# Kernel tuning notes

Measured on AMD Instinct MI355X. Metric: run time of the kernel, lower is better.

## Reference

```python
import jax, jax.numpy as jnp
import numpy as np

TEMPERATURE = 1.0
IGNORE_INDEX = -100


def setup_inputs() -> dict:
    key = jax.random.key(0)
    k1, k2, k3 = jax.random.split(key, 3)
    N, V = 8192, 32000
    Q, D = 8192, 512
    return {
        "input": jax.random.normal(k1, (N, V), dtype=jnp.float32),
        "label": jax.random.randint(k2, (N,), 0, V, dtype=jnp.int64),
        "query": jax.random.normal(k3, (Q, D), dtype=jnp.float32),
    }


def _cross_entropy(logits, label):
    # nn.CrossEntropyLoss(ignore_index=IGNORE_INDEX): mean NLL over non-ignored.
    logp = jax.nn.log_softmax(logits, axis=-1)
    safe_label = jnp.clip(label, 0, logits.shape[-1] - 1)
    nll = -jnp.take_along_axis(logp, safe_label[:, None], axis=-1)[:, 0]
    valid = (label != IGNORE_INDEX)
    num_valid = jnp.maximum(jnp.sum(valid), 1)
    return jnp.sum(jnp.where(valid, nll, 0.0)) / num_valid.astype(logits.dtype)


def _query_similarity_penalty(query, temperature):
    sq_norm = jnp.sum(query * query, axis=-1)  # [Q]
    sq = sq_norm[:, None] + sq_norm[None, :] - 2.0 * (query @ query.T)
    sq = jnp.maximum(sq, 0.0)
    dist = jnp.sqrt(jnp.where(sq > 0.0, sq, 1.0))
    dist = jnp.where(sq > 0.0, dist, 0.0)  # exact 0 on diagonal
    sim = jnp.exp(-dist / temperature)
    return jnp.sqrt(jnp.sum(sim * sim))  # Frobenius norm


def reference(input, label, query):
    ce = _cross_entropy(input, label)
    penalty = _query_similarity_penalty(query, TEMPERATURE)
    return ce + penalty
```

## Files before the change

### kernel.cpp

```cpp
#include <hip/hip_runtime.h>
#include <hip/hip_bf16.h>
#include <cstdint>

typedef unsigned short u16;
typedef __attribute__((ext_vector_type(8))) short short8;
typedef __attribute__((ext_vector_type(4))) float floatx4;

#define IGNORE_INDEX (-100)

#define SIM_OFF 64
#define NLL_OFF 320
#define CNT_OFF 576

__global__ __launch_bounds__(256) void init_acc(float* acc) {
    for (int i = threadIdx.x; i < 1024; i += 256) acc[i] = 0.f;
}

__global__ __launch_bounds__(256) void prep_kernel(const float* __restrict__ q,
                                                   u16* __restrict__ qb,
                                                   float* __restrict__ nrm) {
    const int gwave = (blockIdx.x * 256 + threadIdx.x) >> 6;
    const int lane  = threadIdx.x & 63;
    const float4* src = (const float4*)(q + (size_t)gwave * 512);
    float4 a = src[lane * 2];
    float4 b = src[lane * 2 + 1];
    float v[8] = {a.x, a.y, a.z, a.w, b.x, b.y, b.z, b.w};
    float ss = 0.f;
    union { u16 u[8]; uint4 p; } pk;
#pragma unroll
    for (int t = 0; t < 8; ++t) {
        ss += v[t] * v[t];
        __hip_bfloat16 h = __float2bfloat16(v[t]);
        pk.u[t] = *(u16*)&h;
    }
    ((uint4*)qb)[(size_t)gwave * 64 + lane] = pk.p;
#pragma unroll
    for (int off = 32; off; off >>= 1) ss += __shfl_down(ss, off);
    if (lane == 0) nrm[gwave] = ss;
}

#define GLD16(g, l) __builtin_amdgcn_global_load_lds(                          \
    (const __attribute__((address_space(1))) void*)(g),                        \
    (__attribute__((address_space(3))) void*)(l), 16, 0, 0)

__global__ __launch_bounds__(256, 3) void fused_kernel(const u16* __restrict__ qb,
                                                       const float* __restrict__ nrm,
                                                       const float* __restrict__ x,
                                                       const int* __restrict__ lab,
                                                       float* __restrict__ accs,
                                                       int V, int N, int tiles_per_side) {
    __shared__ __align__(16) u16 At[128 * 64];
    __shared__ __align__(16) u16 Bt[128 * 64];
    __shared__ float red[4];
    const int bid  = blockIdx.x;
    const int tid  = threadIdx.x;
    const int lane = tid & 63;
    const int w    = tid >> 6;
    const int slot = (bid & 63) * 4;

    if (bid % 5 == 0) {
        int t = bid / 5;
        int ti = 0, rem = t;
        while (rem >= tiles_per_side - ti) { rem -= tiles_per_side - ti; ++ti; }
        const int tj = ti + rem;
        const int i0 = ti * 128;
        const int j0 = tj * 128;
        const int wr = w >> 1, wc = w & 1;
        const int m15 = lane & 15, quad = lane >> 4;

        floatx4 acc[4][4];
#pragma unroll
        for (int a = 0; a < 4; ++a)
#pragma unroll
            for (int b = 0; b < 4; ++b) acc[a][b] = (floatx4)0.f;

        for (int kt = 0; kt < 8; ++kt) {
            const int k0 = kt * 64;
#pragma unroll
            for (int it = 0; it < 4; ++it) {
                int c   = it * 256 + tid;
                int row = c >> 3;
                int kc  = (c & 7) ^ (row & 7);
                const u16* ga = qb + (size_t)(i0 + row) * 512 + k0 + kc * 8;
                const u16* gb = qb + (size_t)(j0 + row) * 512 + k0 + kc * 8;
                GLD16(ga, &At[c * 8]);
                GLD16(gb, &Bt[c * 8]);
            }
            __syncthreads();
#pragma unroll
            for (int ks = 0; ks < 2; ++ks) {
                const int kcq = ks * 4 + quad;
                short8 af[4], bfr[4];
#pragma unroll
                for (int f = 0; f < 4; ++f) {
                    int ra = wr * 64 + f * 16 + m15;
                    af[f]  = *(const short8*)&At[(ra * 8 + (kcq ^ (ra & 7))) * 8];
                    int rb = wc * 64 + f * 16 + m15;
                    bfr[f] = *(const short8*)&Bt[(rb * 8 + (kcq ^ (rb & 7))) * 8];
                }
#pragma unroll
                for (int fi = 0; fi < 4; ++fi)
#pragma unroll
                    for (int fj = 0; fj < 4; ++fj)
                        acc[fi][fj] = __builtin_amdgcn_mfma_f32_16x16x32_bf16(
                            af[fi], bfr[fj], acc[fi][fj], 0, 0, 0);
            }
            __syncthreads();
        }

        float ni[4][4], nj[4];
#pragma unroll
        for (int fi = 0; fi < 4; ++fi)
#pragma unroll
            for (int r = 0; r < 4; ++r)
                ni[fi][r] = nrm[i0 + wr * 64 + fi * 16 + quad * 4 + r];
#pragma unroll
        for (int fj = 0; fj < 4; ++fj) nj[fj] = nrm[j0 + wc * 64 + fj * 16 + m15];

        float lsum = 0.f;
#pragma unroll
        for (int fi = 0; fi < 4; ++fi) {
#pragma unroll
            for (int fj = 0; fj < 4; ++fj) {
#pragma unroll
                for (int r = 0; r < 4; ++r) {
                    int i = i0 + wr * 64 + fi * 16 + quad * 4 + r;
                    int j = j0 + wc * 64 + fj * 16 + m15;
                    float sq = ni[fi][r] + nj[fj] - 2.f * acc[fi][fj][r];
                    float s;
                    if (i == j) s = 1.f;
                    else if (sq > 0.f) s = __expf(-sqrtf(sq));
                    else s = 1.f;
                    lsum += s * s;
                }
            }
        }
#pragma unroll
        for (int off = 32; off; off >>= 1) lsum += __shfl_down(lsum, off);
        if (lane == 0) red[w] = lsum;
        __syncthreads();
        if (tid == 0) {
            const float wgt = (ti == tj) ? 1.f : 2.f;
            atomicAdd(&accs[SIM_OFF + slot], wgt * (red[0] + red[1] + red[2] + red[3]));
        }
    } else {
        const int row = bid - bid / 5 - 1;
        if (row >= N) return;
        const float* xr = x + (size_t)row * V;

        int l = 0; float xl = 0.f;
        if (tid == 0) {
            l = lab[row];
            if (l != IGNORE_INDEX) xl = xr[l];
        }

        const int nvec = V >> 2;
        const floatx4* __restrict__ xv = (const floatx4*)xr;
        const int rot = (row * 787) % nvec;
        float s0 = 0.f, s1 = 0.f, s2 = 0.f, s3 = 0.f;

        const int nfull = nvec / 2048;
        for (int k = 0; k < nfull; ++k) {
            floatx4 v[8];
#pragma unroll
            for (int u = 0; u < 8; ++u) {
                int vi = k * 2048 + u * 256 + tid;
                int r  = vi + rot; if (r >= nvec) r -= nvec;
                v[u] = __builtin_nontemporal_load(xv + r);
            }
#pragma unroll
            for (int u = 0; u < 8; ++u) {
                s0 += __expf(v[u].x);
                s1 += __expf(v[u].y);
                s2 += __expf(v[u].z);
                s3 += __expf(v[u].w);
            }
        }
        {
            const int base = nfull * 2048;
            floatx4 v[8];
#pragma unroll
            for (int u = 0; u < 8; ++u) {
                int vb = base + u * 256;
                if (vb < nvec) {
                    int vi = vb + tid;
                    int r  = vi + rot;
                    if (r >= nvec) r -= nvec;
                    if (r >= nvec) r -= nvec;
                    v[u] = __builtin_nontemporal_load(xv + r);
                } else v[u] = (floatx4)0.f;
            }
#pragma unroll
            for (int u = 0; u < 8; ++u) {
                int vb = base + u * 256;
                if (vb < nvec) {
                    int vi = vb + tid;
                    float e0 = __expf(v[u].x), e1 = __expf(v[u].y);
                    float e2 = __expf(v[u].z), e3 = __expf(v[u].w);
                    bool ok = vi < nvec;
                    s0 += ok ? e0 : 0.f;
                    s1 += ok ? e1 : 0.f;
                    s2 += ok ? e2 : 0.f;
                    s3 += ok ? e3 : 0.f;
                }
            }
        }
        float s = (s0 + s1) + (s2 + s3);
#pragma unroll
        for (int off = 32; off; off >>= 1) s += __shfl_down(s, off);
        if (lane == 0) red[w] = s;
        __syncthreads();
        if (tid == 0) {
            float S = red[0] + red[1] + red[2] + red[3];
            if (l != IGNORE_INDEX) {
                atomicAdd(&accs[NLL_OFF + slot], __logf(S) - xl);
                atomicAdd(&accs[CNT_OFF + slot], 1.f);
            }
        }
    }
}

__global__ __launch_bounds__(64) void finalize_kernel(const float* __restrict__ accs,
                                                      float* __restrict__ out) {
    const int t = threadIdx.x;
    float sim = accs[SIM_OFF + t * 4];
    float nll = accs[NLL_OFF + t * 4];
    float cnt = accs[CNT_OFF + t * 4];
#pragma unroll
    for (int off = 32; off; off >>= 1) {
        sim += __shfl_down(sim, off);
        nll += __shfl_down(nll, off);
        cnt += __shfl_down(cnt, off);
    }
    if (t == 0) out[0] = nll / fmaxf(cnt, 1.f) + sqrtf(sim);
}

extern "C" void kernel_launch(void* const* d_in, const int* in_sizes, int n_in,
                              void* d_out, int out_size, void* d_ws, size_t ws_size,
                              hipStream_t stream) {
    const float* input = (const float*)d_in[0];
    const int*   label = (const int*)d_in[1];
    const float* query = (const float*)d_in[2];
    float* out = (float*)d_out;

    const int N = in_sizes[1];
    const int V = in_sizes[0] / N;
    const int D = 512;
    const int Q = in_sizes[2] / D;
    const int T = Q / 128;
    const int U = T * (T + 1) / 2;

    float* accs = (float*)d_ws;
    float* nrm  = (float*)((char*)d_ws + 4096);
    u16*   qb   = (u16*)  ((char*)d_ws + 4096 + 64 * 1024);

    hipLaunchKernelGGL(init_acc, dim3(1), dim3(256), 0, stream, accs);
    hipLaunchKernelGGL(prep_kernel, dim3(Q / 4), dim3(256), 0, stream, query, qb, nrm);
    hipLaunchKernelGGL(fused_kernel, dim3(U * 5), dim3(256), 0, stream,
                       qb, nrm, input, label, accs, V, N, T);
    hipLaunchKernelGGL(finalize_kernel, dim3(1), dim3(64), 0, stream, accs, out);
}
```

Baseline: 1.285 ms.

## Split fused gram/cross-entropy kernel into two separate sequential kernels

The interleaved kernel, which gave every fifth block to the Gram tile and the rest to a cross-entropy row, is split into a gram_kernel launched over the upper-triangle tiles and a ce_kernel launched over rows. Each kernel now gets its own occupancy hint (2 for the Gram kernel, 6 for CE), and the CE loads switch from nontemporal to ordinary loads. This removes register and LDS pressure that the MFMA path forced on the memory-bound CE path. The cost is that the two workloads run one after the other instead of overlapping compute and bandwidth within a single launch.

New measurement: 1.359 ms. +5.8%, slower.

```diff
diff --git a/kernel.cpp b/kernel.cpp
--- a/kernel.cpp
+++ b/kernel.cpp
@@ -43,12 +43,10 @@
     (const __attribute__((address_space(1))) void*)(g),                        \
     (__attribute__((address_space(3))) void*)(l), 16, 0, 0)
 
-__global__ __launch_bounds__(256, 3) void fused_kernel(const u16* __restrict__ qb,
-                                                       const float* __restrict__ nrm,
-                                                       const float* __restrict__ x,
-                                                       const int* __restrict__ lab,
-                                                       float* __restrict__ accs,
-                                                       int V, int N, int tiles_per_side) {
+__global__ __launch_bounds__(256, 2) void gram_kernel(const u16* __restrict__ qb,
+                                                      const float* __restrict__ nrm,
+                                                      float* __restrict__ accs,
+                                                      int tiles_per_side) {
     __shared__ __align__(16) u16 At[128 * 64];
     __shared__ __align__(16) u16 Bt[128 * 64];
     __shared__ float red[4];
@@ -58,164 +56,170 @@
     const int w    = tid >> 6;
     const int slot = (bid & 63) * 4;
 
-    if (bid % 5 == 0) {
-        int t = bid / 5;
-        int ti = 0, rem = t;
-        while (rem >= tiles_per_side - ti) { rem -= tiles_per_side - ti; ++ti; }
-        const int tj = ti + rem;
-        const int i0 = ti * 128;
-        const int j0 = tj * 128;
-        const int wr = w >> 1, wc = w & 1;
-        const int m15 = lane & 15, quad = lane >> 4;
-
-        floatx4 acc[4][4];
-#pragma unroll
-        for (int a = 0; a < 4; ++a)
-#pragma unroll
-            for (int b = 0; b < 4; ++b) acc[a][b] = (floatx4)0.f;
-
-        for (int kt = 0; kt < 8; ++kt) {
-            const int k0 = kt * 64;
-#pragma unroll
-            for (int it = 0; it < 4; ++it) {
-                int c   = it * 256 + tid;
-                int row = c >> 3;
-                int kc  = (c & 7) ^ (row & 7);
-                const u16* ga = qb + (size_t)(i0 + row) * 512 + k0 + kc * 8;
-                const u16* gb = qb + (size_t)(j0 + row) * 512 + k0 + kc * 8;
-                GLD16(ga, &At[c * 8]);
-                GLD16(gb, &Bt[c * 8]);
+    int ti = 0, rem = bid;
+    while (rem >= tiles_per_side - ti) { rem -= tiles_per_side - ti; ++ti; }
+    const int tj = ti + rem;
+    const int i0 = ti * 128;
+    const int j0 = tj * 128;
+    const int wr = w >> 1, wc = w & 1;
+    const int m15 = lane & 15, quad = lane >> 4;
+
+    floatx4 acc[4][4];
+#pragma unroll
+    for (int a = 0; a < 4; ++a)
+#pragma unroll
+        for (int b = 0; b < 4; ++b) acc[a][b] = (floatx4)0.f;
+
+    for (int kt = 0; kt < 8; ++kt) {
+        const int k0 = kt * 64;
+#pragma unroll
+        for (int it = 0; it < 4; ++it) {
+            int c   = it * 256 + tid;
+            int row = c >> 3;
+            int kc  = (c & 7) ^ (row & 7);
+            const u16* ga = qb + (size_t)(i0 + row) * 512 + k0 + kc * 8;
+            const u16* gb = qb + (size_t)(j0 + row) * 512 + k0 + kc * 8;
+            GLD16(ga, &At[c * 8]);
+            GLD16(gb, &Bt[c * 8]);
+        }
+        __syncthreads();
+#pragma unroll
+        for (int ks = 0; ks < 2; ++ks) {
+            const int kcq = ks * 4 + quad;
+            short8 af[4], bfr[4];
+#pragma unroll
+            for (int f = 0; f < 4; ++f) {
+                int ra = wr * 64 + f * 16 + m15;
+                af[f]  = *(const short8*)&At[(ra * 8 + (kcq ^ (ra & 7))) * 8];
+                int rb = wc * 64 + f * 16 + m15;
+                bfr[f] = *(const short8*)&Bt[(rb * 8 + (kcq ^ (rb & 7))) * 8];
             }
-            __syncthreads();
-#pragma unroll
-            for (int ks = 0; ks < 2; ++ks) {
-                const int kcq = ks * 4 + quad;
-                short8 af[4], bfr[4];
-#pragma unroll
-                for (int f = 0; f < 4; ++f) {
-                    int ra = wr * 64 + f * 16 + m15;
-                    af[f]  = *(const short8*)&At[(ra * 8 + (kcq ^ (ra & 7))) * 8];
-                    int rb = wc * 64 + f * 16 + m15;
-                    bfr[f] = *(const short8*)&Bt[(rb * 8 + (kcq ^ (rb & 7))) * 8];
-                }
-#pragma unroll
-                for (int fi = 0; fi < 4; ++fi)
-#pragma unroll
-                    for (int fj = 0; fj < 4; ++fj)
-                        acc[fi][fj] = __builtin_amdgcn_mfma_f32_16x16x32_bf16(
-                            af[fi], bfr[fj], acc[fi][fj], 0, 0, 0);
+#pragma unroll
+            for (int fi = 0; fi < 4; ++fi)
+#pragma unroll
+                for (int fj = 0; fj < 4; ++fj)
+                    acc[fi][fj] = __builtin_amdgcn_mfma_f32_16x16x32_bf16(
+                        af[fi], bfr[fj], acc[fi][fj], 0, 0, 0);
+        }
+        __syncthreads();
+    }
+
+    float ni[4][4], nj[4];
+#pragma unroll
+    for (int fi = 0; fi < 4; ++fi)
+#pragma unroll
+        for (int r = 0; r < 4; ++r)
+            ni[fi][r] = nrm[i0 + wr * 64 + fi * 16 + quad * 4 + r];
+#pragma unroll
+    for (int fj = 0; fj < 4; ++fj) nj[fj] = nrm[j0 + wc * 64 + fj * 16 + m15];
+
+    float lsum = 0.f;
+#pragma unroll
+    for (int fi = 0; fi < 4; ++fi) {
+#pragma unroll
+        for (int fj = 0; fj < 4; ++fj) {
+#pragma unroll
+            for (int r = 0; r < 4; ++r) {
+                int i = i0 + wr * 64 + fi * 16 + quad * 4 + r;
+                int j = j0 + wc * 64 + fj * 16 + m15;
+                float sq = ni[fi][r] + nj[fj] - 2.f * acc[fi][fj][r];
+                float s;
+                if (i == j) s = 1.f;
+                else if (sq > 0.f) s = __expf(-sqrtf(sq));
+                else s = 1.f;
+                lsum += s * s;
             }
-            __syncthreads();
-        }
-
-        float ni[4][4], nj[4];
-#pragma unroll
-        for (int fi = 0; fi < 4; ++fi)
-#pragma unroll
-            for (int r = 0; r < 4; ++r)
-                ni[fi][r] = nrm[i0 + wr * 64 + fi * 16 + quad * 4 + r];
-#pragma unroll
-        for (int fj = 0; fj < 4; ++fj) nj[fj] = nrm[j0 + wc * 64 + fj * 16 + m15];
-
-        float lsum = 0.f;
-#pragma unroll
-        for (int fi = 0; fi < 4; ++fi) {
-#pragma unroll
-            for (int fj = 0; fj < 4; ++fj) {
-#pragma unroll
-                for (int r = 0; r < 4; ++r) {
-                    int i = i0 + wr * 64 + fi * 16 + quad * 4 + r;
-                    int j = j0 + wc * 64 + fj * 16 + m15;
-                    float sq = ni[fi][r] + nj[fj] - 2.f * acc[fi][fj][r];
-                    float s;
-                    if (i == j) s = 1.f;
-                    else if (sq > 0.f) s = __expf(-sqrtf(sq));
-                    else s = 1.f;
-                    lsum += s * s;
-                }
+        }
+    }
+#pragma unroll
+    for (int off = 32; off; off >>= 1) lsum += __shfl_down(lsum, off);
+    if (lane == 0) red[w] = lsum;
+    __syncthreads();
+    if (tid == 0) {
+        const float wgt = (ti == tj) ? 1.f : 2.f;
+        atomicAdd(&accs[SIM_OFF + slot], wgt * (red[0] + red[1] + red[2] + red[3]));
+    }
+}
+
+__global__ __launch_bounds__(256, 6) void ce_kernel(const float* __restrict__ x,
+                                                    const int* __restrict__ lab,
+                                                    float* __restrict__ accs,
+                                                    int V) {
+    __shared__ float red[4];
+    const int row  = blockIdx.x;
+    const int tid  = threadIdx.x;
+    const int lane = tid & 63;
+    const int w    = tid >> 6;
+    const int slot = (row & 63) * 4;
+    const float* xr = x + (size_t)row * V;
+
+    int l = 0; float xl = 0.f;
+    if (tid == 0) {
+        l = lab[row];
+        if (l != IGNORE_INDEX) xl = xr[l];
+    }
+
+    const int nvec = V >> 2;
+    const floatx4* xv = (const floatx4*)xr;
+    const int rot = (row * 787) % nvec;
+    float s0 = 0.f, s1 = 0.f, s2 = 0.f, s3 = 0.f;
+
+    const int nfull = nvec / 2048;
+    for (int k = 0; k < nfull; ++k) {
+        floatx4 v[8];
+#pragma unroll
+        for (int u = 0; u < 8; ++u) {
+            int vi = k * 2048 + u * 256 + tid;
+            int r  = vi + rot; if (r >= nvec) r -= nvec;
+            v[u] = xv[r];
+        }
+#pragma unroll
+        for (int u = 0; u < 8; ++u) {
+            s0 += __expf(v[u].x);
+            s1 += __expf(v[u].y);
+            s2 += __expf(v[u].z);
+            s3 += __expf(v[u].w);
+        }
+    }
+    {
+        const int base = nfull * 2048;
+        floatx4 v[8];
+#pragma unroll
+        for (int u = 0; u < 8; ++u) {
+            int vb = base + u * 256;
+            if (vb < nvec) {
+                int vi = vb + tid;
+                int r  = vi + rot;
+                if (r >= nvec) r -= nvec;
+                if (r >= nvec) r -= nvec;
+                v[u] = xv[r];
+            } else v[u] = (floatx4)0.f;
+        }
+#pragma unroll
+        for (int u = 0; u < 8; ++u) {
+            int vb = base + u * 256;
+            if (vb < nvec) {
+                int vi = vb + tid;
+                float e0 = __expf(v[u].x), e1 = __expf(v[u].y);
+                float e2 = __expf(v[u].z), e3 = __expf(v[u].w);
+                bool ok = vi < nvec;
+                s0 += ok ? e0 : 0.f;
+                s1 += ok ? e1 : 0.f;
+                s2 += ok ? e2 : 0.f;
+                s3 += ok ? e3 : 0.f;
             }
         }
-#pragma unroll
-        for (int off = 32; off; off >>= 1) lsum += __shfl_down(lsum, off);
-        if (lane == 0) red[w] = lsum;
-        __syncthreads();
-        if (tid == 0) {
-            const float wgt = (ti == tj) ? 1.f : 2.f;
-            atomicAdd(&accs[SIM_OFF + slot], wgt * (red[0] + red[1] + red[2] + red[3]));
-        }
-    } else {
-        const int row = bid - bid / 5 - 1;
-        if (row >= N) return;
-        const float* xr = x + (size_t)row * V;
-
-        int l = 0; float xl = 0.f;
-        if (tid == 0) {
-            l = lab[row];
-            if (l != IGNORE_INDEX) xl = xr[l];
-        }
-
-        const int nvec = V >> 2;
-        const floatx4* __restrict__ xv = (const floatx4*)xr;
-        const int rot = (row * 787) % nvec;
-        float s0 = 0.f, s1 = 0.f, s2 = 0.f, s3 = 0.f;
-
-        const int nfull = nvec / 2048;
-        for (int k = 0; k < nfull; ++k) {
-            floatx4 v[8];
-#pragma unroll
-            for (int u = 0; u < 8; ++u) {
-                int vi = k * 2048 + u * 256 + tid;
-                int r  = vi + rot; if (r >= nvec) r -= nvec;
-                v[u] = __builtin_nontemporal_load(xv + r);
-            }
-#pragma unroll
-            for (int u = 0; u < 8; ++u) {
-                s0 += __expf(v[u].x);
-                s1 += __expf(v[u].y);
-                s2 += __expf(v[u].z);
-                s3 += __expf(v[u].w);
-            }
-        }
-        {
-            const int base = nfull * 2048;
-            floatx4 v[8];
-#pragma unroll
-            for (int u = 0; u < 8; ++u) {
-                int vb = base + u * 256;
-                if (vb < nvec) {
-                    int vi = vb + tid;
-                    int r  = vi + rot;
-                    if (r >= nvec) r -= nvec;
-                    if (r >= nvec) r -= nvec;
-                    v[u] = __builtin_nontemporal_load(xv + r);
-                } else v[u] = (floatx4)0.f;
-            }
-#pragma unroll
-            for (int u = 0; u < 8; ++u) {
-                int vb = base + u * 256;
-                if (vb < nvec) {
-                    int vi = vb + tid;
-                    float e0 = __expf(v[u].x), e1 = __expf(v[u].y);
-                    float e2 = __expf(v[u].z), e3 = __expf(v[u].w);
-                    bool ok = vi < nvec;
-                    s0 += ok ? e0 : 0.f;
-                    s1 += ok ? e1 : 0.f;
-                    s2 += ok ? e2 : 0.f;
-                    s3 += ok ? e3 : 0.f;
-                }
-            }
-        }
-        float s = (s0 + s1) + (s2 + s3);
-#pragma unroll
-        for (int off = 32; off; off >>= 1) s += __shfl_down(s, off);
-        if (lane == 0) red[w] = s;
-        __syncthreads();
-        if (tid == 0) {
-            float S = red[0] + red[1] + red[2] + red[3];
-            if (l != IGNORE_INDEX) {
-                atomicAdd(&accs[NLL_OFF + slot], __logf(S) - xl);
-                atomicAdd(&accs[CNT_OFF + slot], 1.f);
-            }
+    }
+    float s = (s0 + s1) + (s2 + s3);
+#pragma unroll
+    for (int off = 32; off; off >>= 1) s += __shfl_down(s, off);
+    if (lane == 0) red[w] = s;
+    __syncthreads();
+    if (tid == 0) {
+        float S = red[0] + red[1] + red[2] + red[3];
+        if (l != IGNORE_INDEX) {
+            atomicAdd(&accs[NLL_OFF + slot], __logf(S) - xl);
+            atomicAdd(&accs[CNT_OFF + slot], 1.f);
         }
     }
 }
@@ -256,7 +260,7 @@
 
     hipLaunchKernelGGL(init_acc, dim3(1), dim3(256), 0, stream, accs);
     hipLaunchKernelGGL(prep_kernel, dim3(Q / 4), dim3(256), 0, stream, query, qb, nrm);
-    hipLaunchKernelGGL(fused_kernel, dim3(U * 5), dim3(256), 0, stream,
-                       qb, nrm, input, label, accs, V, N, T);
+    hipLaunchKernelGGL(gram_kernel, dim3(U), dim3(256), 0, stream, qb, nrm, accs, T);
+    hipLaunchKernelGGL(ce_kernel, dim3(N), dim3(256), 0, stream, input, label, accs, V);
     hipLaunchKernelGGL(finalize_kernel, dim3(1), dim3(64), 0, stream, accs, out);
 }
```
